# Performance work log

Measured on AMD Instinct MI355X. Metric: run time of the kernel, lower is better.

## Reference

```python
import jax, jax.numpy as jnp
import numpy as np

B, L, D, DP = 64, 4096, 512, 64


def setup_inputs() -> dict:
    key = jax.random.key(0)
    ks = jax.random.split(key, 7)
    s = 0.02
    return {
        "source": jax.random.normal(ks[0], (B, D), jnp.float32),
        "main_embs": jax.random.normal(ks[1], (L, B, D), jnp.float32),   # time-major memory bank
        "pos_embs": jax.random.normal(ks[2], (L, B, DP), jnp.float32),
        "W_main_in": jax.random.normal(ks[3], (D, D), jnp.float32) * s,  # main_scorer.linear_in (no bias)
        "W_pos_in": jax.random.normal(ks[4], (D, DP), jnp.float32) * s,  # pos_scorer.linear_in (no bias)
        "W_out": jax.random.normal(ks[5], (D, 2 * D), jnp.float32) * s,  # linear_out (no bias, attn_type!='mlp')
        "memory_lengths": jnp.maximum(jax.random.randint(ks[6], (B,), 1, L + 1), 1),
    }


def reference(source, main_embs, pos_embs, W_main_in, W_pos_in, W_out, memory_lengths):
    # to batch-major: (B, L, D) / (B, L, DP)
    me = jnp.transpose(main_embs, (1, 0, 2))
    pe = jnp.transpose(pos_embs, (1, 0, 2))

    # 'general' scorer: project context then dot with query (qrs_len == 1)
    mc = jnp.einsum("bld,ed->ble", me, W_main_in)          # (B, L, D)
    main_align = jnp.einsum("bd,bld->bl", source, mc)      # (B, L)
    pc = jnp.einsum("blp,dp->bld", pe, W_pos_in)           # (B, L, D)
    pos_align = jnp.einsum("bd,bld->bl", source, pc)       # (B, L)

    # length mask + softmax on each branch
    mask = jnp.arange(me.shape[1])[None, :] < memory_lengths[:, None]  # (B, L)
    neg_inf = jnp.float32(-jnp.inf)
    ma = jax.nn.softmax(jnp.where(mask, main_align, neg_inf), axis=-1)
    pa = jax.nn.softmax(jnp.where(mask, pos_align, neg_inf), axis=-1)

    # elementwise combine + renormalize
    av = ma * pa
    av = av / jnp.sum(av, axis=-1, keepdims=True)

    # context vector + output projection + tanh
    c_t = jnp.einsum("bl,bld->bd", av, me)                 # (B, D)
    concat_c = jnp.concatenate([c_t, source], axis=-1)     # (B, 2D)
    attn_h = jnp.tanh(concat_c @ W_out.T)                  # (B, D)

    return attn_h, av, ma, pa
```

## Files before the change

kernel.cpp:

```cpp
#include <hip/hip_runtime.h>
#include <cstddef>

#define NB 64
#define NL 4096
#define ND 512
#define NDP 64
#define LC 64
#define NLC (NL / LC)
#define NSLOT 4096

typedef float v2f __attribute__((ext_vector_type(2)));

__device__ __forceinline__ v2f fma2(v2f a, v2f b, v2f c) {
    return __builtin_elementwise_fma(a, b, c);
}

__global__ void __launch_bounds__(128) queries_plan_kernel(
    const float* __restrict__ source, const float* __restrict__ Wmi,
    const float* __restrict__ Wpi, const int* __restrict__ lens,
    float* __restrict__ qpm, float* __restrict__ qpp,
    int* __restrict__ table)
{
    if (blockIdx.x == NB * 4) {
        if (threadIdx.x < 64) {
            const int lane = threadIdx.x;
            const int nc = (lens[lane] + LC - 1) >> 6;
            int pre = nc;
            #pragma unroll
            for (int off = 1; off < 64; off <<= 1) {
                const int v = __shfl_up(pre, off);
                if (lane >= off) pre += v;
            }
            const int start = pre - nc;
            for (int j = 0; j < nc; ++j) table[start + j] = (lane << 6) | j;
            const int T = __shfl(pre, 63);
            for (int s = T + lane; s < NSLOT; s += 64) table[s] = -1;
        }
        return;
    }

    __shared__ float s[128];
    const int b  = blockIdx.x >> 2;
    const int eq = blockIdx.x & 3;
    const int t  = threadIdx.x;
    const int e0 = eq * 128;
    s[t] = source[b * ND + e0 + t];
    __syncthreads();

    const int d0 = t * 4;
    float4 a0 = {0,0,0,0}, a1 = {0,0,0,0};
    #pragma unroll 4
    for (int e = 0; e < 128; e += 2) {
        const float4 w0 = *(const float4*)(Wmi + (size_t)(e0 + e) * ND + d0);
        const float4 w1 = *(const float4*)(Wmi + (size_t)(e0 + e + 1) * ND + d0);
        const float x0 = s[e], x1 = s[e + 1];
        a0.x = fmaf(x0, w0.x, a0.x); a0.y = fmaf(x0, w0.y, a0.y);
        a0.z = fmaf(x0, w0.z, a0.z); a0.w = fmaf(x0, w0.w, a0.w);
        a1.x = fmaf(x1, w1.x, a1.x); a1.y = fmaf(x1, w1.y, a1.y);
        a1.z = fmaf(x1, w1.z, a1.z); a1.w = fmaf(x1, w1.w, a1.w);
    }
    a0.x += a1.x; a0.y += a1.y; a0.z += a1.z; a0.w += a1.w;
    *(float4*)(qpm + (size_t)(b * 4 + eq) * ND + d0) = a0;

    if (t < NDP) {
        float c0 = 0.f, c1 = 0.f;
        #pragma unroll 4
        for (int e = 0; e < 128; e += 2) {
            c0 = fmaf(s[e],     Wpi[(size_t)(e0 + e) * NDP + t],     c0);
            c1 = fmaf(s[e + 1], Wpi[(size_t)(e0 + e + 1) * NDP + t], c1);
        }
        qpp[(b * 4 + eq) * NDP + t] = c0 + c1;
    }
}

__global__ void __launch_bounds__(256, 4) pass1_kernel(
    const float* __restrict__ me, const float* __restrict__ pe,
    const float* __restrict__ qpm, const float* __restrict__ qpp,
    const int* __restrict__ mem_len, const int* __restrict__ table,
    float* __restrict__ a_main, float* __restrict__ a_pos,
    float* __restrict__ Sbuf, float* __restrict__ MZ)
{
    __shared__ __align__(16) float qp_lds[4][NDP];
    const int lane = threadIdx.x & 63;
    const int wid  = threadIdx.x >> 6;
    const int task = table[blockIdx.x * 4 + wid];
    if (task < 0) return;
    const int b  = task >> 6;
    const int lc = task & 63;

    const int len  = mem_len[b];
    const int l0   = lc * LC;
    const int nrow = min(LC, len - l0);
    const int nr4  = (nrow + 3) & ~3;
    const int last = nrow - 1;

    float4 q0 = {0,0,0,0}, q1 = {0,0,0,0};
    float qp = 0.f;
    #pragma unroll
    for (int eq = 0; eq < 4; ++eq) {
        const float4* qr = (const float4*)(qpm + (size_t)(b * 4 + eq) * ND);
        const float4 u0 = qr[lane], u1 = qr[64 + lane];
        q0.x += u0.x; q0.y += u0.y; q0.z += u0.z; q0.w += u0.w;
        q1.x += u1.x; q1.y += u1.y; q1.z += u1.z; q1.w += u1.w;
        qp += qpp[(b * 4 + eq) * NDP + lane];
    }
    qp_lds[wid][lane] = qp;

    float accp = 0.f;
    {
        const int prow = l0 + (lane & 31) ? l0 + (lane & 63) : l0;
    }
    {
        const int prow = l0 + min(lane, last);
        const float4* pr = (const float4*)(pe + ((size_t)prow * NB + b) * NDP);
        #pragma unroll
        for (int k = 0; k < 16; ++k) {
            const float4 pv = pr[k];
            const float4 qv = *(const float4*)&qp_lds[wid][k * 4];
            accp = fmaf(pv.x, qv.x, accp);
            accp = fmaf(pv.y, qv.y, accp);
            accp = fmaf(pv.z, qv.z, accp);
            accp = fmaf(pv.w, qv.w, accp);
        }
        if (lane < nrow) a_pos[(size_t)b * NL + l0 + lane] = accp;
    }
    const int accp_i = __float_as_int(accp);

    const size_t rstride = (size_t)NB * ND;
    const float* base = me + ((size_t)l0 * NB + b) * ND;

    float m = -1e30f, Z = 0.f, keep = 0.f;
    v2f S0 = {0,0}, S1 = {0,0}, S2 = {0,0}, S3 = {0,0};

    float4 A[4][2], B[4][2];

    auto process = [&](float4 R[4][2], int i0) {
        float acc[4];
        #pragma unroll
        for (int j = 0; j < 4; ++j) {
            v2f dd = {0.f, 0.f};
            dd = fma2((v2f){R[j][0].x, R[j][0].y}, (v2f){q0.x, q0.y}, dd);
            dd = fma2((v2f){R[j][0].z, R[j][0].w}, (v2f){q0.z, q0.w}, dd);
            dd = fma2((v2f){R[j][1].x, R[j][1].y}, (v2f){q1.x, q1.y}, dd);
            dd = fma2((v2f){R[j][1].z, R[j][1].w}, (v2f){q1.z, q1.w}, dd);
            acc[j] = dd.x + dd.y;
        }
        #pragma unroll
        for (int off = 32; off; off >>= 1) {
            #pragma unroll
            for (int j = 0; j < 4; ++j)
                acc[j] += __shfl_xor(acc[j], off);
        }
        #pragma unroll
        for (int j = 0; j < 4; ++j) {
            const int row = i0 + j;
            keep = (lane == row) ? acc[j] : keep;
            const float ap = __int_as_float(
                __builtin_amdgcn_readlane(accp_i, min(row, last)));
            const float sv = (row < nrow) ? acc[j] + ap : -1e30f;
            if (sv > m) {
                const float sc = __expf(m - sv);
                const v2f sc2 = {sc, sc};
                Z = fmaf(Z, sc, 1.f);
                S0 = fma2(S0, sc2, (v2f){R[j][0].x, R[j][0].y});
                S1 = fma2(S1, sc2, (v2f){R[j][0].z, R[j][0].w});
                S2 = fma2(S2, sc2, (v2f){R[j][1].x, R[j][1].y});
                S3 = fma2(S3, sc2, (v2f){R[j][1].z, R[j][1].w});
                m = sv;
            } else {
                const float w = __expf(sv - m);
                const v2f w2 = {w, w};
                Z += w;
                S0 = fma2((v2f){R[j][0].x, R[j][0].y}, w2, S0);
                S1 = fma2((v2f){R[j][0].z, R[j][0].w}, w2, S1);
                S2 = fma2((v2f){R[j][1].x, R[j][1].y}, w2, S2);
                S3 = fma2((v2f){R[j][1].z, R[j][1].w}, w2, S3);
            }
        }
    };

    #pragma unroll
    for (int j = 0; j < 4; ++j) {
        const float* p = base + (size_t)min(j, last) * rstride;
        A[j][0] = ((const float4*)p)[lane];
        A[j][1] = ((const float4*)p)[64 + lane];
    }

    int i = 0;
    for (;;) {
        #pragma unroll
        for (int j = 0; j < 4; ++j) {
            const float* p = base + (size_t)min(i + 4 + j, last) * rstride;
            B[j][0] = ((const float4*)p)[lane];
            B[j][1] = ((const float4*)p)[64 + lane];
        }
        process(A, i);
        i += 4;
        if (i >= nr4) break;

        #pragma unroll
        for (int j = 0; j < 4; ++j) {
            const float* p = base + (size_t)min(i + 4 + j, last) * rstride;
            A[j][0] = ((const float4*)p)[lane];
            A[j][1] = ((const float4*)p)[64 + lane];
        }
        process(B, i);
        i += 4;
        if (i >= nr4) break;
    }

    if (lane < nrow) a_main[(size_t)b * NL + l0 + lane] = keep;

    float* sp = Sbuf + ((size_t)b * NLC + lc) * ND;
    ((float4*)sp)[lane]      = (float4){S0.x, S0.y, S1.x, S1.y};
    ((float4*)sp)[64 + lane] = (float4){S2.x, S2.y, S3.x, S3.y};
    if (lane == 0) {
        MZ[2 * (b * NLC + lc)]     = m;
        MZ[2 * (b * NLC + lc) + 1] = Z;
    }
}

__global__ void __launch_bounds__(1024) stats_ctx_kernel(
    const float* __restrict__ MZ, const float* __restrict__ Sbuf,
    const int* __restrict__ mem_len,
    float* __restrict__ ma_io, float* __restrict__ pa_io,
    float* __restrict__ out_av, float* __restrict__ c_t)
{
    __shared__ float red[16][6];
    __shared__ float bc[6];
    __shared__ float coef_s[NLC];
    const int b = blockIdx.x;
    const int tid = threadIdx.x;
    const int lane = tid & 63, wid = tid >> 6;
    const int len = mem_len[b];

    float va[4], vp[4];
    float Am = -1e30f, Pm = -1e30f, Cm = -1e30f;
    #pragma unroll
    for (int k = 0; k < 4; ++k) {
        const int l = tid + k * 1024;
        va[k] = ma_io[(size_t)b * NL + l];
        vp[k] = pa_io[(size_t)b * NL + l];
        if (l < len) {
            Am = fmaxf(Am, va[k]);
            Pm = fmaxf(Pm, vp[k]);
            Cm = fmaxf(Cm, va[k] + vp[k]);
        }
    }
    #pragma unroll
    for (int off = 32; off; off >>= 1) {
        Am = fmaxf(Am, __shfl_xor(Am, off));
        Pm = fmaxf(Pm, __shfl_xor(Pm, off));
        Cm = fmaxf(Cm, __shfl_xor(Cm, off));
    }
    if (lane == 0) { red[wid][0] = Am; red[wid][1] = Pm; red[wid][2] = Cm; }
    __syncthreads();
    if (tid < 16) {
        float a = red[tid][0], p = red[tid][1], c = red[tid][2];
        #pragma unroll
        for (int off = 8; off; off >>= 1) {
            a = fmaxf(a, __shfl_xor(a, off));
            p = fmaxf(p, __shfl_xor(p, off));
            c = fmaxf(c, __shfl_xor(c, off));
        }
        if (tid == 0) { bc[0] = a; bc[1] = p; bc[2] = c; }
    }
    __syncthreads();
    const float MA = bc[0], MP = bc[1], MC = bc[2];

    float Az = 0.f, Pz = 0.f, Cz = 0.f;
    #pragma unroll
    for (int k = 0; k < 4; ++k) {
        const int l = tid + k * 1024;
        if (l < len) {
            Az += __expf(va[k] - MA);
            Pz += __expf(vp[k] - MP);
            Cz += __expf(va[k] + vp[k] - MC);
        }
    }
    #pragma unroll
    for (int off = 32; off; off >>= 1) {
        Az += __shfl_xor(Az, off);
        Pz += __shfl_xor(Pz, off);
        Cz += __shfl_xor(Cz, off);
    }
    if (lane == 0) { red[wid][3] = Az; red[wid][4] = Pz; red[wid][5] = Cz; }
    __syncthreads();
    if (tid < 16) {
        float a = red[tid][3], p = red[tid][4], c = red[tid][5];
        #pragma unroll
        for (int off = 8; off; off >>= 1) {
            a += __shfl_xor(a, off);
            p += __shfl_xor(p, off);
            c += __shfl_xor(c, off);
        }
        if (tid == 0) { bc[3] = a; bc[4] = p; bc[5] = c; }
    }
    __syncthreads();
    const float iA = 1.f / bc[3], iP = 1.f / bc[4], iC = 1.f / bc[5];
    const int nv = (len + LC - 1) >> 6;

    if (tid < NLC) {
        const float mlc = MZ[2 * (b * NLC + tid)];
        coef_s[tid] = (tid < nv) ? __expf(mlc - MC) * iC : 0.f;
    }

    #pragma unroll
    for (int k = 0; k < 4; ++k) {
        const int l = tid + k * 1024;
        const bool v = l < len;
        const size_t idx = (size_t)b * NL + l;
        ma_io[idx]  = v ? __expf(va[k] - MA) * iA : 0.f;
        pa_io[idx]  = v ? __expf(vp[k] - MP) * iP : 0.f;
        out_av[idx] = v ? __expf(va[k] + vp[k] - MC) * iC : 0.f;
    }
    __syncthreads();

    if (tid < 128) {
        float4 acc = {0.f, 0.f, 0.f, 0.f};
        for (int lcc = 0; lcc < nv; ++lcc) {
            const float cf = coef_s[lcc];
            const float4 sv4 =
                ((const float4*)(Sbuf + ((size_t)b * NLC + lcc) * ND))[tid];
            acc.x = fmaf(cf, sv4.x, acc.x);
            acc.y = fmaf(cf, sv4.y, acc.y);
            acc.z = fmaf(cf, sv4.z, acc.z);
            acc.w = fmaf(cf, sv4.w, acc.w);
        }
        ((float4*)(c_t + b * ND))[tid] = acc;
    }
}

__global__ void __launch_bounds__(256) out_kernel(
    const float* __restrict__ c_t, const float* __restrict__ source,
    const float* __restrict__ Wout, float* __restrict__ attn_h)
{
    __shared__ float cs[2 * ND];
    const int b = blockIdx.x >> 3;
    const int eg = blockIdx.x & 7;
    const int tid = threadIdx.x;

    for (int d = tid; d < ND; d += 256) {
        cs[d] = c_t[b * ND + d];
        cs[ND + d] = source[b * ND + d];
    }
    __syncthreads();

    const int wid = tid >> 6, lane = tid & 63;
    const float4* csv = (const float4*)cs;
    for (int e = eg * 64 + wid; e < eg * 64 + 64; e += 4) {
        const float4* wrow = (const float4*)(Wout + (size_t)e * 2 * ND);
        float acc = 0.f;
        #pragma unroll
        for (int j = 0; j < 4; ++j) {
            const float4 w = wrow[lane + 64 * j];
            const float4 c = csv[lane + 64 * j];
            acc += w.x * c.x + w.y * c.y + w.z * c.z + w.w * c.w;
        }
        #pragma unroll
        for (int off = 32; off; off >>= 1) acc += __shfl_xor(acc, off);
        if (lane == 0) attn_h[(size_t)b * ND + e] = tanhf(acc);
    }
}

extern "C" void kernel_launch(void* const* d_in, const int* in_sizes, int n_in,
                              void* d_out, int out_size, void* d_ws, size_t ws_size,
                              hipStream_t stream)
{
    const float* source = (const float*)d_in[0];
    const float* me     = (const float*)d_in[1];
    const float* pe     = (const float*)d_in[2];
    const float* Wmi    = (const float*)d_in[3];
    const float* Wpi    = (const float*)d_in[4];
    const float* Wout   = (const float*)d_in[5];
    const int*   lens   = (const int*)d_in[6];

    float* out    = (float*)d_out;
    float* attn_h = out;
    float* av     = attn_h + NB * ND;
    float* ma     = av + NB * NL;
    float* pa     = ma + NB * NL;

    float* ws    = (float*)d_ws;
    float* qpm   = ws;
    float* qpp   = qpm + NB * 4 * ND;
    float* Sbuf  = qpp + NB * 4 * NDP;
    float* MZ    = Sbuf + (size_t)NB * NLC * ND;
    float* c_t   = MZ + NB * NLC * 2;
    int*   table = (int*)(c_t + NB * ND);

    queries_plan_kernel<<<NB * 4 + 1, 128, 0, stream>>>(source, Wmi, Wpi,
                                                        lens, qpm, qpp, table);
    pass1_kernel       <<<NSLOT / 4, 256, 0, stream>>>(me, pe, qpm, qpp, lens,
                                                       table, ma, pa, Sbuf, MZ);
    stats_ctx_kernel   <<<NB, 1024, 0, stream>>>(MZ, Sbuf, lens, ma, pa, av, c_t);
    out_kernel         <<<NB * 8, 256, 0, stream>>>(c_t, source, Wout, attn_h);
}
```

Measured before the change: 115.2 us.

## Fuse output projection into stats kernel and interleave chunk work table

The output projection (c_t concatenated with source, multiplied by W_out, then tanh) moves into the stats/context kernel, so c_t stays in shared memory and one kernel launch plus the global c_t round trip go away. Only 64 blocks now do the W_out GEMV, each reading all of W_out, where before 512 blocks shared that work. This may lengthen the tail. The planning table is also rebuilt with ballots, so chunk j of every batch is placed together instead of batch-contiguous, interleaving batches across pass1 slots for better load balance.

```diff
diff --git a/kernel.cpp b/kernel.cpp
--- a/kernel.cpp
+++ b/kernel.cpp
@@ -22,18 +22,31 @@
     int* __restrict__ table)
 {
     if (blockIdx.x == NB * 4) {
-        if (threadIdx.x < 64) {
-            const int lane = threadIdx.x;
+        __shared__ unsigned long long masks[64];
+        __shared__ int excl_lds[64];
+        const int tid = threadIdx.x;
+        if (tid < 64) {
+            const int lane = tid;
             const int nc = (lens[lane] + LC - 1) >> 6;
-            int pre = nc;
+            for (int lc = 0; lc < 64; ++lc) {
+                const unsigned long long m = __ballot(nc > lc);
+                if (lane == lc) masks[lc] = m;
+            }
+            const int cnt = __popcll(masks[lane]);
+            int incl = cnt;
             #pragma unroll
             for (int off = 1; off < 64; off <<= 1) {
-                const int v = __shfl_up(pre, off);
-                if (lane >= off) pre += v;
+                const int v = __shfl_up(incl, off);
+                if (lane >= off) incl += v;
             }
-            const int start = pre - nc;
-            for (int j = 0; j < nc; ++j) table[start + j] = (lane << 6) | j;
-            const int T = __shfl(pre, 63);
+            excl_lds[lane] = incl - cnt;
+            const int T = __shfl(incl, 63);
+            const unsigned long long below = ((1ull << lane) - 1ull);
+            for (int j = 0; j < nc; ++j) {
+                const int excl = excl_lds[j];
+                const int rank = __popcll(masks[j] & below);
+                table[excl + rank] = (lane << 6) | j;
+            }
             for (int s = T + lane; s < NSLOT; s += 64) table[s] = -1;
         }
         return;
@@ -107,9 +120,6 @@
     qp_lds[wid][lane] = qp;
 
     float accp = 0.f;
-    {
-        const int prow = l0 + (lane & 31) ? l0 + (lane & 63) : l0;
-    }
     {
         const int prow = l0 + min(lane, last);
         const float4* pr = (const float4*)(pe + ((size_t)prow * NB + b) * NDP);
@@ -220,15 +230,17 @@
     }
 }
 
-__global__ void __launch_bounds__(1024) stats_ctx_kernel(
+__global__ void __launch_bounds__(1024) tail_kernel(
     const float* __restrict__ MZ, const float* __restrict__ Sbuf,
-    const int* __restrict__ mem_len,
+    const int* __restrict__ mem_len, const float* __restrict__ source,
+    const float* __restrict__ Wout,
     float* __restrict__ ma_io, float* __restrict__ pa_io,
-    float* __restrict__ out_av, float* __restrict__ c_t)
+    float* __restrict__ out_av, float* __restrict__ attn_h)
 {
     __shared__ float red[16][6];
     __shared__ float bc[6];
     __shared__ float coef_s[NLC];
+    __shared__ __align__(16) float cs[2 * ND];
     const int b = blockIdx.x;
     const int tid = threadIdx.x;
     const int lane = tid & 63, wid = tid >> 6;
@@ -304,6 +316,7 @@
         const float mlc = MZ[2 * (b * NLC + tid)];
         coef_s[tid] = (tid < nv) ? __expf(mlc - MC) * iC : 0.f;
     }
+    if (tid >= 512) cs[ND + (tid - 512)] = source[b * ND + (tid - 512)];
 
     #pragma unroll
     for (int k = 0; k < 4; ++k) {
@@ -327,28 +340,12 @@
             acc.z = fmaf(cf, sv4.z, acc.z);
             acc.w = fmaf(cf, sv4.w, acc.w);
         }
-        ((float4*)(c_t + b * ND))[tid] = acc;
-    }
-}
-
-__global__ void __launch_bounds__(256) out_kernel(
-    const float* __restrict__ c_t, const float* __restrict__ source,
-    const float* __restrict__ Wout, float* __restrict__ attn_h)
-{
-    __shared__ float cs[2 * ND];
-    const int b = blockIdx.x >> 3;
-    const int eg = blockIdx.x & 7;
-    const int tid = threadIdx.x;
-
-    for (int d = tid; d < ND; d += 256) {
-        cs[d] = c_t[b * ND + d];
-        cs[ND + d] = source[b * ND + d];
-    }
-    __syncthreads();
-
-    const int wid = tid >> 6, lane = tid & 63;
+        ((float4*)cs)[tid] = acc;
+    }
+    __syncthreads();
+
     const float4* csv = (const float4*)cs;
-    for (int e = eg * 64 + wid; e < eg * 64 + 64; e += 4) {
+    for (int e = wid; e < ND; e += 16) {
         const float4* wrow = (const float4*)(Wout + (size_t)e * 2 * ND);
         float acc = 0.f;
         #pragma unroll
@@ -386,13 +383,12 @@
     float* qpp   = qpm + NB * 4 * ND;
     float* Sbuf  = qpp + NB * 4 * NDP;
     float* MZ    = Sbuf + (size_t)NB * NLC * ND;
-    float* c_t   = MZ + NB * NLC * 2;
-    int*   table = (int*)(c_t + NB * ND);
+    int*   table = (int*)(MZ + NB * NLC * 2);
 
     queries_plan_kernel<<<NB * 4 + 1, 128, 0, stream>>>(source, Wmi, Wpi,
                                                         lens, qpm, qpp, table);
     pass1_kernel       <<<NSLOT / 4, 256, 0, stream>>>(me, pe, qpm, qpp, lens,
                                                        table, ma, pa, Sbuf, MZ);
-    stats_ctx_kernel   <<<NB, 1024, 0, stream>>>(MZ, Sbuf, lens, ma, pa, av, c_t);
-    out_kernel         <<<NB * 8, 256, 0, stream>>>(c_t, source, Wout, attn_h);
-}
+    tail_kernel        <<<NB, 1024, 0, stream>>>(MZ, Sbuf, lens, source, Wout,
+                                                 ma, pa, av, attn_h);
+}
```

New measurement: 114.1 us. Within noise of the previous version (-1.0%).
